# Kernel tuning notes

Measured on AMD Instinct MI355X. Metric: run time of the kernel, lower is better.

The kernel has to match this reference:

```python
import jax, jax.numpy as jnp
import numpy as np

EMBED_DIM = 1024
NUM_HEADS = 16
HEAD_DIM = EMBED_DIM // NUM_HEADS
B, S = 2, 2048


def setup_inputs() -> dict:
    key = jax.random.key(0)
    ks = jax.random.split(key, 9)
    scale = 1.0 / np.sqrt(EMBED_DIM)
    return {
        "x": jax.random.normal(ks[0], (B, S, EMBED_DIM), dtype=jnp.float32),
        "Wq": jax.random.normal(ks[1], (EMBED_DIM, EMBED_DIM), dtype=jnp.float32) * scale,
        "bq": jnp.zeros((EMBED_DIM,), dtype=jnp.float32),
        "Wk": jax.random.normal(ks[2], (EMBED_DIM, EMBED_DIM), dtype=jnp.float32) * scale,
        "bk": jnp.zeros((EMBED_DIM,), dtype=jnp.float32),
        "Wv": jax.random.normal(ks[3], (EMBED_DIM, EMBED_DIM), dtype=jnp.float32) * scale,
        "bv": jnp.zeros((EMBED_DIM,), dtype=jnp.float32),
        "Wo": jax.random.normal(ks[4], (EMBED_DIM, EMBED_DIM), dtype=jnp.float32) * scale,
        "bo": jnp.zeros((EMBED_DIM,), dtype=jnp.float32),
    }


def _split_heads(t):
    # [B, S, E] -> [B, H, S, Dh]
    b, s, _ = t.shape
    return t.reshape(b, s, NUM_HEADS, HEAD_DIM).transpose(0, 2, 1, 3)


def reference(x, Wq, bq, Wk, bk, Wv, bv, Wo, bo):
    q = _split_heads(x @ Wq + bq)
    k = _split_heads(x @ Wk + bk)
    v = _split_heads(x @ Wv + bv)
    scale = jnp.sqrt(jnp.asarray(HEAD_DIM, dtype=x.dtype))
    scores = jnp.einsum("bhqd,bhkd->bhqk", q, k) / scale
    attn = jax.nn.softmax(scores, axis=-1)
    out = jnp.einsum("bhqk,bhkd->bhqd", attn, v)  # [B,H,S,Dh]
    out = out.transpose(0, 2, 1, 3).reshape(x.shape[0], x.shape[1], EMBED_DIM)
    return out @ Wo + bo
```

## Files before the change

kernel.cpp:

```cpp
#include <hip/hip_runtime.h>
#include <math.h>
#include <stdint.h>

typedef __bf16 bf16;
typedef __bf16 bf16x2 __attribute__((ext_vector_type(2)));
typedef __bf16 bf16x4 __attribute__((ext_vector_type(4)));
typedef __bf16 bf16x8 __attribute__((ext_vector_type(8)));
typedef float f32x4 __attribute__((ext_vector_type(4)));
typedef float f32x16 __attribute__((ext_vector_type(16)));

constexpr int E = 1024;
constexpr int S = 2048;
constexpr int H = 16;


__device__ __forceinline__ void gload16(const void* g, void* l) {
  __builtin_amdgcn_global_load_lds(
      (__attribute__((address_space(1))) void*)(uintptr_t)g,
      (__attribute__((address_space(3))) void*)(uint32_t)(uintptr_t)l, 16, 0, 0);
}

__device__ __forceinline__ f32x4 mfma16(bf16x8 a, bf16x8 b, f32x4 c) {
  return __builtin_amdgcn_mfma_f32_16x16x32_bf16(a, b, c, 0, 0, 0);
}
__device__ __forceinline__ f32x16 mfma32(bf16x8 a, bf16x8 b, f32x16 c) {
  return __builtin_amdgcn_mfma_f32_32x32x16_bf16(a, b, c, 0, 0, 0);
}

__device__ __forceinline__ float fexp2(float x) {
#if __has_builtin(__builtin_amdgcn_exp2f)
  return __builtin_amdgcn_exp2f(x);
#else
  float r;
  asm("v_exp_f32 %0, %1" : "=v"(r) : "v"(x));
  return r;
#endif
}

__device__ __forceinline__ uint32_t pkbf(float lo, float hi) {
  bf16x2 p;
  p[0] = (bf16)lo;
  p[1] = (bf16)hi;
  return __builtin_bit_cast(uint32_t, p);
}

__global__ __launch_bounds__(256) void cast_x(const float* __restrict__ x,
                                              bf16* __restrict__ o) {
  const size_t i = ((size_t)blockIdx.x * 256 + threadIdx.x) * 8;
  const float4 a = *(const float4*)(x + i);
  const float4 b = *(const float4*)(x + i + 4);
  bf16x8 r;
  r[0] = (bf16)a.x; r[1] = (bf16)a.y; r[2] = (bf16)a.z; r[3] = (bf16)a.w;
  r[4] = (bf16)b.x; r[5] = (bf16)b.y; r[6] = (bf16)b.z; r[7] = (bf16)b.w;
  *(bf16x8*)(o + i) = r;
}

__global__ __launch_bounds__(256) void transpose_cast_w(
    const float* __restrict__ W0, const float* __restrict__ W1,
    const float* __restrict__ W2, const float* __restrict__ W3,
    bf16* __restrict__ T0, bf16* __restrict__ T1, bf16* __restrict__ T2,
    bf16* __restrict__ T3) {
  const float* W;
  bf16* T;
  switch (blockIdx.z) {
    case 0: W = W0; T = T0; break;
    case 1: W = W1; T = T1; break;
    case 2: W = W2; T = T2; break;
    default: W = W3; T = T3; break;
  }
  __shared__ float t[64][65];
  const int k0 = blockIdx.y * 64, n0 = blockIdx.x * 64;
  const int tr = threadIdx.x >> 4;
  const int tc = (threadIdx.x & 15) * 4;
#pragma unroll
  for (int u = 0; u < 4; ++u) {
    const float4 v = *(const float4*)(W + (size_t)(k0 + tr + u * 16) * E + n0 + tc);
    t[tr + u * 16][tc + 0] = v.x;
    t[tr + u * 16][tc + 1] = v.y;
    t[tr + u * 16][tc + 2] = v.z;
    t[tr + u * 16][tc + 3] = v.w;
  }
  __syncthreads();
#pragma unroll
  for (int u = 0; u < 4; ++u) {
    const int n = tr + u * 16;
    bf16x4 o;
#pragma unroll
    for (int i = 0; i < 4; ++i) o[i] = (bf16)t[tc + i][n];
    *(bf16x4*)(T + (size_t)(n0 + n) * E + k0 + tc) = o;
  }
}

__global__ __launch_bounds__(256) void gemm_qkv(const bf16* __restrict__ A,
                                                const bf16* __restrict__ Wt,
                                                const float* __restrict__ bq,
                                                const float* __restrict__ bk,
                                                const float* __restrict__ bv,
                                                bf16* __restrict__ qo,
                                                bf16* __restrict__ ko,
                                                bf16* __restrict__ vo) {
  __shared__ __attribute__((aligned(16))) bf16 Asm[128 * 32];
  __shared__ __attribute__((aligned(16))) bf16 Bsm[128 * 32];
  const int z = blockIdx.z;
  const bf16* Bt = Wt + (size_t)z * E * E;
  const float* bias = (z == 0) ? bq : (z == 1) ? bk : bv;
  const int tid = threadIdx.x;
  const int w = tid >> 6, lane = tid & 63, quad = lane >> 4, ln = lane & 15;
  const int bm = blockIdx.y * 128, bn = blockIdx.x * 128;
  const int wr = w >> 1, wc = w & 1;
  const int srow = w * 32 + (lane >> 2);
  const int scol = (lane & 3) * 8;
  const bf16* Ag = A + (size_t)(bm + srow) * E + scol;
  const bf16* Bg = Bt + (size_t)(bn + srow) * E + scol;
  f32x4 acc[4][4] = {};

  for (int k0 = 0; k0 < E; k0 += 32) {
    gload16(Ag + k0, &Asm[(w * 32) * 32]);
    gload16(Ag + k0 + (size_t)16 * E, &Asm[(w * 32 + 16) * 32]);
    gload16(Bg + k0, &Bsm[(w * 32) * 32]);
    gload16(Bg + k0 + (size_t)16 * E, &Bsm[(w * 32 + 16) * 32]);
    __syncthreads();
    bf16x8 af[4], bfr[4];
#pragma unroll
    for (int t = 0; t < 4; ++t) {
      af[t] = *(const bf16x8*)&Asm[(wr * 64 + t * 16 + ln) * 32 + quad * 8];
      bfr[t] = *(const bf16x8*)&Bsm[(wc * 64 + t * 16 + ln) * 32 + quad * 8];
    }
#pragma unroll
    for (int rt = 0; rt < 4; ++rt)
#pragma unroll
      for (int ct = 0; ct < 4; ++ct)
        acc[rt][ct] = mfma16(af[rt], bfr[ct], acc[rt][ct]);
    __syncthreads();
  }

  const float scl = (z == 0) ? 0.18033688f : 1.0f;
  const int hglob = (bn + wc * 64) >> 6;
  float bvv[4];
#pragma unroll
  for (int ct = 0; ct < 4; ++ct) bvv[ct] = bias[bn + wc * 64 + ct * 16 + ln];

#pragma unroll
  for (int rt = 0; rt < 4; ++rt) {
    const int row0 = bm + wr * 64 + rt * 16 + quad * 4;
    const int bb = row0 >> 11;
    const int rl = row0 & 2047;
    const size_t hb = (size_t)(bb * 16 + hglob) * 131072;
#pragma unroll
    for (int ct = 0; ct < 4; ++ct) {
      if (z == 2) {
        const int mt = ct >> 1, ln32 = ((ct & 1) << 4) | ln;
        const int tau = rl >> 6, hfv = (rl >> 3) & 1, j0 = rl & 7;
        bf16x4 p;
#pragma unroll
        for (int r = 0; r < 4; ++r) p[r] = (bf16)(acc[rt][ct][r] + bvv[ct]);
        *(bf16x4*)&vo[hb + (size_t)((tau * 8 + mt * 4 + rt) * 512 +
                                    hfv * 256 + ln32 * 8 + j0)] = p;
      } else {
        bf16* o = (z == 0) ? qo : ko;
        const int t = rl >> 5, ln0 = rl & 31;
        const size_t base =
            hb + (size_t)((t * 4 + ct) * 512 + (ln >> 3) * 256 + (ln & 7));
#pragma unroll
        for (int r = 0; r < 4; ++r)
          o[base + (ln0 + r) * 8] = (bf16)((acc[rt][ct][r] + bvv[ct]) * scl);
      }
    }
  }
}

__global__ __launch_bounds__(256) void gemm_wo(const bf16* __restrict__ A,
                                               const bf16* __restrict__ Bt,
                                               const float* __restrict__ bias,
                                               float* __restrict__ C) {
  __shared__ __attribute__((aligned(16))) bf16 Asm[64 * 32];
  __shared__ __attribute__((aligned(16))) bf16 Bsm[128 * 32];
  const int tid = threadIdx.x;
  const int w = tid >> 6, lane = tid & 63, quad = lane >> 4, ln = lane & 15;
  const int bm = blockIdx.y * 64, bn = blockIdx.x * 128;
  const int wr = w >> 1, wc = w & 1;
  const int sr = lane >> 2, sc = (lane & 3) * 8;
  const bf16* Ag = A + (size_t)(bm + w * 16 + sr) * E + sc;
  const bf16* Bg = Bt + (size_t)(bn + w * 32 + sr) * E + sc;
  f32x4 acc[2][4] = {};

  for (int k0 = 0; k0 < E; k0 += 32) {
    gload16(Ag + k0, &Asm[(w * 16) * 32]);
    gload16(Bg + k0, &Bsm[(w * 32) * 32]);
    gload16(Bg + k0 + (size_t)16 * E, &Bsm[(w * 32 + 16) * 32]);
    __syncthreads();
    bf16x8 af[2], bfr[4];
#pragma unroll
    for (int t = 0; t < 2; ++t)
      af[t] = *(const bf16x8*)&Asm[(wr * 32 + t * 16 + ln) * 32 + quad * 8];
#pragma unroll
    for (int t = 0; t < 4; ++t)
      bfr[t] = *(const bf16x8*)&Bsm[(wc * 64 + t * 16 + ln) * 32 + quad * 8];
#pragma unroll
    for (int rt = 0; rt < 2; ++rt)
#pragma unroll
      for (int ct = 0; ct < 4; ++ct)
        acc[rt][ct] = mfma16(af[rt], bfr[ct], acc[rt][ct]);
    __syncthreads();
  }

  float bvv[4];
#pragma unroll
  for (int ct = 0; ct < 4; ++ct) bvv[ct] = bias[bn + wc * 64 + ct * 16 + ln];
#pragma unroll
  for (int rt = 0; rt < 2; ++rt) {
    const int row0 = bm + wr * 32 + rt * 16 + quad * 4;
#pragma unroll
    for (int ct = 0; ct < 4; ++ct) {
      const int c = bn + wc * 64 + ct * 16 + ln;
#pragma unroll
      for (int r = 0; r < 4; ++r)
        C[(size_t)(row0 + r) * E + c] = acc[rt][ct][r] + bvv[ct];
    }
  }
}

__global__ __launch_bounds__(512, 4) void attn_mfma(const bf16* __restrict__ Qf,
                                                    const bf16* __restrict__ Kf,
                                                    const bf16* __restrict__ Vf,
                                                    bf16* __restrict__ Og) {
  __shared__ __attribute__((aligned(16))) char smem[65536];

  const int tid = threadIdx.x;
  const int w = tid >> 6, lane = tid & 63, ln = lane & 31, hf = lane >> 5;
  const int qi = w & 3, ki = w >> 2;
  const int tq = blockIdx.x * 4 + qi;
  const int h = blockIdx.y, b = blockIdx.z;
  const size_t fb = (size_t)(b * H + h) * 131072;

  bf16x8 qf[4];
  {
    const bf16* qb = Qf + fb + (size_t)tq * 2048 + lane * 8;
#pragma unroll
    for (int c = 0; c < 4; ++c) qf[c] = *(const bf16x8*)(qb + c * 512);
  }

  const bf16* Ksrc = Kf + fb + qi * 1024 + lane * 8;
  const bf16* Vsrc = Vf + fb + qi * 1024 + lane * 8;
  const int dstoff = ki * 4096 + qi * 1024;

  float lpart = 0.f;
  f32x16 oacc[2] = {};

#define STAGE(i, buf)                                                  \
  do {                                                                 \
    const size_t toff = (size_t)(ki * 16 + (i)) * 4096;                \
    bf16* kd = (bf16*)(smem + (buf) * 32768) + dstoff;                 \
    bf16* vd = (bf16*)(smem + (buf) * 32768 + 16384) + dstoff;         \
    gload16(Ksrc + toff, kd);                                          \
    gload16(Ksrc + toff + 512, kd + 512);                              \
    gload16(Vsrc + toff, vd);                                          \
    gload16(Vsrc + toff + 512, vd + 512);                              \
  } while (0)

  STAGE(0, 0);
  __syncthreads();

#pragma unroll 2
  for (int i = 0; i < 16; ++i) {
    const int cur = i & 1;
    if (i < 15) STAGE(i + 1, cur ^ 1);
    const bf16* Ks = (const bf16*)(smem + cur * 32768) + ki * 4096;
    const bf16* Vs = (const bf16*)(smem + cur * 32768 + 16384) + ki * 4096;

#pragma unroll
    for (int mt = 0; mt < 2; ++mt) {
      f32x16 st = {};
      __builtin_amdgcn_s_setprio(1);
#pragma unroll
      for (int c = 0; c < 4; ++c)
        st = mfma32(*(const bf16x8*)&Ks[(mt * 4 + c) * 512 + lane * 8], qf[c],
                    st);
      __builtin_amdgcn_s_setprio(0);

      float pe[16];
#pragma unroll
      for (int r = 0; r < 16; ++r) {
        pe[r] = fexp2(st[r]);
        lpart += pe[r];
      }

      bf16x8 pb[2];
#pragma unroll
      for (int cl = 0; cl < 2; ++cl) {
        uint32_t a01 = pkbf(pe[cl * 8 + 0], pe[cl * 8 + 1]);
        uint32_t a23 = pkbf(pe[cl * 8 + 2], pe[cl * 8 + 3]);
        uint32_t b01 = pkbf(pe[cl * 8 + 4], pe[cl * 8 + 5]);
        uint32_t b23 = pkbf(pe[cl * 8 + 6], pe[cl * 8 + 7]);
        auto r0 = __builtin_amdgcn_permlane32_swap(a01, b01, false, false);
        auto r1 = __builtin_amdgcn_permlane32_swap(a23, b23, false, false);
        union {
          bf16x8 v;
          uint32_t u[4];
        } pu;
        pu.u[0] = r0[0];
        pu.u[1] = r1[0];
        pu.u[2] = r0[1];
        pu.u[3] = r1[1];
        pb[cl] = pu.v;
      }

      __builtin_amdgcn_s_setprio(1);
#pragma unroll
      for (int vt = 0; vt < 2; ++vt) {
        oacc[vt] = mfma32(
            *(const bf16x8*)&Vs[(vt * 4 + mt * 2 + 0) * 512 + lane * 8], pb[0],
            oacc[vt]);
        oacc[vt] = mfma32(
            *(const bf16x8*)&Vs[(vt * 4 + mt * 2 + 1) * 512 + lane * 8], pb[1],
            oacc[vt]);
      }
      __builtin_amdgcn_s_setprio(0);
    }
    __syncthreads();
  }
#undef STAGE

  float* Ocmb = (float*)smem;
  float* Lcmb = (float*)(smem + 32768);
  if (ki == 1) {
#pragma unroll
    for (int vt = 0; vt < 2; ++vt)
#pragma unroll
      for (int r = 0; r < 16; ++r)
        Ocmb[qi * 2048 + (vt * 16 + r) * 64 + lane] = oacc[vt][r];
    Lcmb[qi * 64 + lane] = lpart;
  }
  __syncthreads();
  if (ki == 0) {
#pragma unroll
    for (int vt = 0; vt < 2; ++vt)
#pragma unroll
      for (int r = 0; r < 16; ++r)
        oacc[vt][r] += Ocmb[qi * 2048 + (vt * 16 + r) * 64 + lane];
    lpart += Lcmb[qi * 64 + lane];

    lpart += __shfl_xor(lpart, 32);
    const float inv = 1.0f / lpart;

    bf16* orow = Og + ((size_t)b * S + (size_t)tq * 32 + ln) * E + h * 64;
#pragma unroll
    for (int vt = 0; vt < 2; ++vt) {
#pragma unroll
      for (int g = 0; g < 4; ++g) {
        bf16x4 o;
#pragma unroll
        for (int j = 0; j < 4; ++j) o[j] = (bf16)(oacc[vt][g * 4 + j] * inv);
        *(bf16x4*)&orow[vt * 32 + g * 8 + hf * 4] = o;
      }
    }
  }
}

extern "C" void kernel_launch(void* const* d_in, const int* in_sizes, int n_in,
                              void* d_out, int out_size, void* d_ws, size_t ws_size,
                              hipStream_t stream) {
  const float* x = (const float*)d_in[0];
  const float* Wq = (const float*)d_in[1];
  const float* bq = (const float*)d_in[2];
  const float* Wk = (const float*)d_in[3];
  const float* bk = (const float*)d_in[4];
  const float* Wv = (const float*)d_in[5];
  const float* bv = (const float*)d_in[6];
  const float* Wo = (const float*)d_in[7];
  const float* bo = (const float*)d_in[8];

  const size_t ME = (size_t)4096 * 1024;
  const size_t WE = (size_t)1024 * 1024;
  bf16* xb = (bf16*)d_ws;
  bf16* wqt = xb + ME;
  bf16* wkt = wqt + WE;
  bf16* wvt = wkt + WE;
  bf16* wot = wvt + WE;
  bf16* qb = wot + WE;
  bf16* kb = qb + ME;
  bf16* vt = kb + ME;
  bf16* ab = vt + ME;

  cast_x<<<2048, 256, 0, stream>>>(x, xb);
  transpose_cast_w<<<dim3(16, 16, 4), 256, 0, stream>>>(Wq, Wk, Wv, Wo, wqt, wkt,
                                                        wvt, wot);
  gemm_qkv<<<dim3(8, 32, 3), 256, 0, stream>>>(xb, wqt, bq, bk, bv, qb, kb, vt);
  attn_mfma<<<dim3(S / 128, H, 2), 512, 0, stream>>>(qb, kb, vt, ab);
  gemm_wo<<<dim3(8, 64), 256, 0, stream>>>(ab, wot, bo, (float*)d_out);
}
```

Before: 189.1 us.

## Give each attention wave two query tiles to reuse K/V LDS fragments

The attention kernel drops from 8 waves to 4 waves per block. Each wave now handles two 32-row query groups, so every K and V fragment read from LDS feeds two MFMAs instead of one. Each thread issues twice as many async global-to-LDS loads to fill the same tiles. The aim is to halve LDS read traffic per unit of compute, at the cost of more registers per wave (two sets of accumulators and Q fragments) and fewer waves available to hide latency.

```diff
diff --git a/kernel.cpp b/kernel.cpp
--- a/kernel.cpp
+++ b/kernel.cpp
@@ -220,7 +220,7 @@
   }
 }
 
-__global__ __launch_bounds__(512, 4) void attn_mfma(const bf16* __restrict__ Qf,
+__global__ __launch_bounds__(256, 2) void attn_mfma(const bf16* __restrict__ Qf,
                                                     const bf16* __restrict__ Kf,
                                                     const bf16* __restrict__ Vf,
                                                     bf16* __restrict__ Og) {
@@ -228,34 +228,35 @@
 
   const int tid = threadIdx.x;
   const int w = tid >> 6, lane = tid & 63, ln = lane & 31, hf = lane >> 5;
-  const int qi = w & 3, ki = w >> 2;
-  const int tq = blockIdx.x * 4 + qi;
+  const int qi = w & 1, ki = w >> 1;
+  const int q64 = blockIdx.x * 2 + qi;
   const int h = blockIdx.y, b = blockIdx.z;
   const size_t fb = (size_t)(b * H + h) * 131072;
 
-  bf16x8 qf[4];
-  {
-    const bf16* qb = Qf + fb + (size_t)tq * 2048 + lane * 8;
-#pragma unroll
-    for (int c = 0; c < 4; ++c) qf[c] = *(const bf16x8*)(qb + c * 512);
-  }
-
-  const bf16* Ksrc = Kf + fb + qi * 1024 + lane * 8;
-  const bf16* Vsrc = Vf + fb + qi * 1024 + lane * 8;
-  const int dstoff = ki * 4096 + qi * 1024;
-
-  float lpart = 0.f;
-  f32x16 oacc[2] = {};
-
-#define STAGE(i, buf)                                                  \
-  do {                                                                 \
-    const size_t toff = (size_t)(ki * 16 + (i)) * 4096;                \
-    bf16* kd = (bf16*)(smem + (buf) * 32768) + dstoff;                 \
-    bf16* vd = (bf16*)(smem + (buf) * 32768 + 16384) + dstoff;         \
-    gload16(Ksrc + toff, kd);                                          \
-    gload16(Ksrc + toff + 512, kd + 512);                              \
-    gload16(Vsrc + toff, vd);                                          \
-    gload16(Vsrc + toff + 512, vd + 512);                              \
+  bf16x8 qf[2][4];
+#pragma unroll
+  for (int qg = 0; qg < 2; ++qg) {
+    const bf16* qb = Qf + fb + (size_t)(q64 * 2 + qg) * 2048 + lane * 8;
+#pragma unroll
+    for (int c = 0; c < 4; ++c) qf[qg][c] = *(const bf16x8*)(qb + c * 512);
+  }
+
+  const bf16* Ksrc = Kf + fb + qi * 2048 + lane * 8;
+  const bf16* Vsrc = Vf + fb + qi * 2048 + lane * 8;
+  const int dstoff = ki * 4096 + qi * 2048;
+
+  float lpart[2] = {0.f, 0.f};
+  f32x16 oacc[2][2] = {};
+
+#define STAGE(i, buf)                                                   \
+  do {                                                                  \
+    const size_t toff = (size_t)(ki * 16 + (i)) * 4096;                 \
+    bf16* kd = (bf16*)(smem + (buf) * 32768) + dstoff;                  \
+    bf16* vd = (bf16*)(smem + (buf) * 32768 + 16384) + dstoff;          \
+    _Pragma("unroll") for (int c = 0; c < 4; ++c) {                     \
+      gload16(Ksrc + toff + c * 512, kd + c * 512);                     \
+      gload16(Vsrc + toff + c * 512, vd + c * 512);                     \
+    }                                                                   \
   } while (0)
 
   STAGE(0, 0);
@@ -270,51 +271,65 @@
 
 #pragma unroll
     for (int mt = 0; mt < 2; ++mt) {
-      f32x16 st = {};
+      bf16x8 kf4[4];
+#pragma unroll
+      for (int c = 0; c < 4; ++c)
+        kf4[c] = *(const bf16x8*)&Ks[(mt * 4 + c) * 512 + lane * 8];
+
+      f32x16 st[2] = {{}, {}};
       __builtin_amdgcn_s_setprio(1);
 #pragma unroll
-      for (int c = 0; c < 4; ++c)
-        st = mfma32(*(const bf16x8*)&Ks[(mt * 4 + c) * 512 + lane * 8], qf[c],
-                    st);
+      for (int c = 0; c < 4; ++c) {
+        st[0] = mfma32(kf4[c], qf[0][c], st[0]);
+        st[1] = mfma32(kf4[c], qf[1][c], st[1]);
+      }
       __builtin_amdgcn_s_setprio(0);
 
-      float pe[16];
-#pragma unroll
-      for (int r = 0; r < 16; ++r) {
-        pe[r] = fexp2(st[r]);
-        lpart += pe[r];
+      bf16x8 pb[2][2];
+#pragma unroll
+      for (int qg = 0; qg < 2; ++qg) {
+        float pe[16];
+#pragma unroll
+        for (int r = 0; r < 16; ++r) {
+          pe[r] = fexp2(st[qg][r]);
+          lpart[qg] += pe[r];
+        }
+#pragma unroll
+        for (int cl = 0; cl < 2; ++cl) {
+          uint32_t a01 = pkbf(pe[cl * 8 + 0], pe[cl * 8 + 1]);
+          uint32_t a23 = pkbf(pe[cl * 8 + 2], pe[cl * 8 + 3]);
+          uint32_t b01 = pkbf(pe[cl * 8 + 4], pe[cl * 8 + 5]);
+          uint32_t b23 = pkbf(pe[cl * 8 + 6], pe[cl * 8 + 7]);
+          auto r0 = __builtin_amdgcn_permlane32_swap(a01, b01, false, false);
+          auto r1 = __builtin_amdgcn_permlane32_swap(a23, b23, false, false);
+          union {
+            bf16x8 v;
+            uint32_t u[4];
+          } pu;
+          pu.u[0] = r0[0];
+          pu.u[1] = r1[0];
+          pu.u[2] = r0[1];
+          pu.u[3] = r1[1];
+          pb[qg][cl] = pu.v;
+        }
       }
 
-      bf16x8 pb[2];
-#pragma unroll
-      for (int cl = 0; cl < 2; ++cl) {
-        uint32_t a01 = pkbf(pe[cl * 8 + 0], pe[cl * 8 + 1]);
-        uint32_t a23 = pkbf(pe[cl * 8 + 2], pe[cl * 8 + 3]);
-        uint32_t b01 = pkbf(pe[cl * 8 + 4], pe[cl * 8 + 5]);
-        uint32_t b23 = pkbf(pe[cl * 8 + 6], pe[cl * 8 + 7]);
-        auto r0 = __builtin_amdgcn_permlane32_swap(a01, b01, false, false);
-        auto r1 = __builtin_amdgcn_permlane32_swap(a23, b23, false, false);
-        union {
-          bf16x8 v;
-          uint32_t u[4];
-        } pu;
-        pu.u[0] = r0[0];
-        pu.u[1] = r1[0];
-        pu.u[2] = r0[1];
-        pu.u[3] = r1[1];
-        pb[cl] = pu.v;
-      }
+      bf16x8 vf[2][2];
+#pragma unroll
+      for (int vt = 0; vt < 2; ++vt)
+#pragma unroll
+        for (int cl = 0; cl < 2; ++cl)
+          vf[vt][cl] =
+              *(const bf16x8*)&Vs[(vt * 4 + mt * 2 + cl) * 512 + lane * 8];
 
       __builtin_amdgcn_s_setprio(1);
 #pragma unroll
-      for (int vt = 0; vt < 2; ++vt) {
-        oacc[vt] = mfma32(
-            *(const bf16x8*)&Vs[(vt * 4 + mt * 2 + 0) * 512 + lane * 8], pb[0],
-            oacc[vt]);
-        oacc[vt] = mfma32(
-            *(const bf16x8*)&Vs[(vt * 4 + mt * 2 + 1) * 512 + lane * 8], pb[1],
-            oacc[vt]);
-      }
+      for (int qg = 0; qg < 2; ++qg)
+#pragma unroll
+        for (int vt = 0; vt < 2; ++vt) {
+          oacc[qg][vt] = mfma32(vf[vt][0], pb[qg][0], oacc[qg][vt]);
+          oacc[qg][vt] = mfma32(vf[vt][1], pb[qg][1], oacc[qg][vt]);
+        }
       __builtin_amdgcn_s_setprio(0);
     }
     __syncthreads();
@@ -325,33 +340,43 @@
   float* Lcmb = (float*)(smem + 32768);
   if (ki == 1) {
 #pragma unroll
-    for (int vt = 0; vt < 2; ++vt)
-#pragma unroll
-      for (int r = 0; r < 16; ++r)
-        Ocmb[qi * 2048 + (vt * 16 + r) * 64 + lane] = oacc[vt][r];
-    Lcmb[qi * 64 + lane] = lpart;
+    for (int qg = 0; qg < 2; ++qg) {
+#pragma unroll
+      for (int vt = 0; vt < 2; ++vt)
+#pragma unroll
+        for (int r = 0; r < 16; ++r)
+          Ocmb[(qi * 2 + qg) * 2048 + (vt * 16 + r) * 64 + lane] =
+              oacc[qg][vt][r];
+      Lcmb[(qi * 2 + qg) * 64 + lane] = lpart[qg];
+    }
   }
   __syncthreads();
   if (ki == 0) {
 #pragma unroll
-    for (int vt = 0; vt < 2; ++vt)
-#pragma unroll
-      for (int r = 0; r < 16; ++r)
-        oacc[vt][r] += Ocmb[qi * 2048 + (vt * 16 + r) * 64 + lane];
-    lpart += Lcmb[qi * 64 + lane];
-
-    lpart += __shfl_xor(lpart, 32);
-    const float inv = 1.0f / lpart;
-
-    bf16* orow = Og + ((size_t)b * S + (size_t)tq * 32 + ln) * E + h * 64;
-#pragma unroll
-    for (int vt = 0; vt < 2; ++vt) {
-#pragma unroll
-      for (int g = 0; g < 4; ++g) {
-        bf16x4 o;
-#pragma unroll
-        for (int j = 0; j < 4; ++j) o[j] = (bf16)(oacc[vt][g * 4 + j] * inv);
-        *(bf16x4*)&orow[vt * 32 + g * 8 + hf * 4] = o;
+    for (int qg = 0; qg < 2; ++qg) {
+#pragma unroll
+      for (int vt = 0; vt < 2; ++vt)
+#pragma unroll
+        for (int r = 0; r < 16; ++r)
+          oacc[qg][vt][r] +=
+              Ocmb[(qi * 2 + qg) * 2048 + (vt * 16 + r) * 64 + lane];
+      float lp = lpart[qg] + Lcmb[(qi * 2 + qg) * 64 + lane];
+
+      lp += __shfl_xor(lp, 32);
+      const float inv = 1.0f / lp;
+
+      bf16* orow =
+          Og + ((size_t)b * S + (size_t)q64 * 64 + qg * 32 + ln) * E + h * 64;
+#pragma unroll
+      for (int vt = 0; vt < 2; ++vt) {
+#pragma unroll
+        for (int g = 0; g < 4; ++g) {
+          bf16x4 o;
+#pragma unroll
+          for (int j = 0; j < 4; ++j)
+            o[j] = (bf16)(oacc[qg][vt][g * 4 + j] * inv);
+          *(bf16x4*)&orow[vt * 32 + g * 8 + hf * 4] = o;
+        }
       }
     }
   }
@@ -386,6 +411,6 @@
   transpose_cast_w<<<dim3(16, 16, 4), 256, 0, stream>>>(Wq, Wk, Wv, Wo, wqt, wkt,
                                                         wvt, wot);
   gemm_qkv<<<dim3(8, 32, 3), 256, 0, stream>>>(xb, wqt, bq, bk, bv, qb, kb, vt);
-  attn_mfma<<<dim3(S / 128, H, 2), 512, 0, stream>>>(qb, kb, vt, ab);
+  attn_mfma<<<dim3(S / 128, H, 2), 256, 0, stream>>>(qb, kb, vt, ab);
   gemm_wo<<<dim3(8, 64), 256, 0, stream>>>(ab, wot, bo, (float*)d_out);
 }
```

Measured after the change: 186.8 us. About the same (-1.2%).

## Load V fragments directly from global into registers, halve LDS footprint

Applied to the files above, without the earlier changes.

V tiles are no longer staged through LDS via async global-to-LDS copies. Each wave loads its V MFMA fragments straight from global memory into registers, issued before the K prefetch and again mid-iteration. This halves shared memory per block, which can raise occupancy and cuts LDS traffic. The row-sum accumulation is also restructured as a tree add to shorten the dependency chain. The trade-off is that global load latency is now exposed inside the loop, and V data is no longer shared across waves in LDS.

```diff
diff --git a/kernel.cpp b/kernel.cpp
--- a/kernel.cpp
+++ b/kernel.cpp
@@ -224,7 +224,7 @@
                                                     const bf16* __restrict__ Kf,
                                                     const bf16* __restrict__ Vf,
                                                     bf16* __restrict__ Og) {
-  __shared__ __attribute__((aligned(16))) char smem[65536];
+  __shared__ __attribute__((aligned(16))) char smem[33792];
 
   const int tid = threadIdx.x;
   const int w = tid >> 6, lane = tid & 63, ln = lane & 31, hf = lane >> 5;
@@ -241,8 +241,8 @@
   }
 
   const bf16* Ksrc = Kf + fb + qi * 1024 + lane * 8;
-  const bf16* Vsrc = Vf + fb + qi * 1024 + lane * 8;
   const int dstoff = ki * 4096 + qi * 1024;
+  const bf16* Vg = Vf + fb + (size_t)ki * 16 * 4096 + lane * 8;
 
   float lpart = 0.f;
   f32x16 oacc[2] = {};
@@ -250,12 +250,9 @@
 #define STAGE(i, buf)                                                  \
   do {                                                                 \
     const size_t toff = (size_t)(ki * 16 + (i)) * 4096;                \
-    bf16* kd = (bf16*)(smem + (buf) * 32768) + dstoff;                 \
-    bf16* vd = (bf16*)(smem + (buf) * 32768 + 16384) + dstoff;         \
+    bf16* kd = (bf16*)(smem + (buf) * 16384) + dstoff;                 \
     gload16(Ksrc + toff, kd);                                          \
     gload16(Ksrc + toff + 512, kd + 512);                              \
-    gload16(Vsrc + toff, vd);                                          \
-    gload16(Vsrc + toff + 512, vd + 512);                              \
   } while (0)
 
   STAGE(0, 0);
@@ -264,12 +261,28 @@
 #pragma unroll 2
   for (int i = 0; i < 16; ++i) {
     const int cur = i & 1;
+    const bf16* vt8 = Vg + (size_t)i * 4096;
+
+    bf16x8 vfr[2][2];
+#pragma unroll
+    for (int vt = 0; vt < 2; ++vt)
+#pragma unroll
+      for (int cl = 0; cl < 2; ++cl)
+        vfr[vt][cl] = *(const bf16x8*)(vt8 + (vt * 4 + 0 * 2 + cl) * 512);
+
     if (i < 15) STAGE(i + 1, cur ^ 1);
-    const bf16* Ks = (const bf16*)(smem + cur * 32768) + ki * 4096;
-    const bf16* Vs = (const bf16*)(smem + cur * 32768 + 16384) + ki * 4096;
+    const bf16* Ks = (const bf16*)(smem + cur * 16384) + ki * 4096;
 
 #pragma unroll
     for (int mt = 0; mt < 2; ++mt) {
+      if (mt == 1) {
+#pragma unroll
+        for (int vt = 0; vt < 2; ++vt)
+#pragma unroll
+          for (int cl = 0; cl < 2; ++cl)
+            vfr[vt][cl] = *(const bf16x8*)(vt8 + (vt * 4 + 2 + cl) * 512);
+      }
+
       f32x16 st = {};
       __builtin_amdgcn_s_setprio(1);
 #pragma unroll
@@ -280,10 +293,11 @@
 
       float pe[16];
 #pragma unroll
-      for (int r = 0; r < 16; ++r) {
-        pe[r] = fexp2(st[r]);
-        lpart += pe[r];
-      }
+      for (int r = 0; r < 16; ++r) pe[r] = fexp2(st[r]);
+      lpart += (((pe[0] + pe[1]) + (pe[2] + pe[3])) +
+                ((pe[4] + pe[5]) + (pe[6] + pe[7]))) +
+               (((pe[8] + pe[9]) + (pe[10] + pe[11])) +
+                ((pe[12] + pe[13]) + (pe[14] + pe[15])));
 
       bf16x8 pb[2];
 #pragma unroll
@@ -308,12 +322,8 @@
       __builtin_amdgcn_s_setprio(1);
 #pragma unroll
       for (int vt = 0; vt < 2; ++vt) {
-        oacc[vt] = mfma32(
-            *(const bf16x8*)&Vs[(vt * 4 + mt * 2 + 0) * 512 + lane * 8], pb[0],
-            oacc[vt]);
-        oacc[vt] = mfma32(
-            *(const bf16x8*)&Vs[(vt * 4 + mt * 2 + 1) * 512 + lane * 8], pb[1],
-            oacc[vt]);
+        oacc[vt] = mfma32(vfr[vt][0], pb[0], oacc[vt]);
+        oacc[vt] = mfma32(vfr[vt][1], pb[1], oacc[vt]);
       }
       __builtin_amdgcn_s_setprio(0);
     }
```

After: 213.1 us. +12.7%, slower.
